# Kernel tuning notes

Hardware: AMD Instinct MI355X
Metric: run time of the kernel (lower is better)

The kernel has to match this reference:

```python
import jax, jax.numpy as jnp
import numpy as np

N_NODES = 100000
N_EDGES = 1600000
IN_FEATS = 128
HIDDEN = 150
NUM_OUT = 128


def setup_inputs() -> dict:
    key = jax.random.key(0)
    ks = jax.random.split(key, 9)
    x = jax.random.normal(ks[0], (N_NODES, IN_FEATS), dtype=jnp.float32)
    src = jax.random.randint(ks[1], (N_EDGES,), 0, N_NODES, dtype=jnp.int32)
    dst = jax.random.randint(ks[2], (N_EDGES,), 0, N_NODES, dtype=jnp.int32)
    def lin(k, fan_in, fan_out):
        bound = 1.0 / np.sqrt(fan_in)
        return jax.random.uniform(k, (fan_in, fan_out), jnp.float32, -bound, bound)
    W_self1 = lin(ks[3], IN_FEATS, HIDDEN)
    W_neigh1 = lin(ks[4], IN_FEATS, HIDDEN)
    b1 = jnp.zeros((HIDDEN,), jnp.float32)
    W_self2 = lin(ks[5], HIDDEN, NUM_OUT)
    W_neigh2 = lin(ks[6], HIDDEN, NUM_OUT)
    b2 = jnp.zeros((NUM_OUT,), jnp.float32)
    return {"x": x, "src": src, "dst": dst,
            "W_self1": W_self1, "W_neigh1": W_neigh1, "b1": b1,
            "W_self2": W_self2, "W_neigh2": W_neigh2, "b2": b2}


def _mean_agg(h, src, dst, deg_inv):
    # segment-mean of source features onto destination nodes; isolated nodes -> 0
    summed = jax.ops.segment_sum(h[src], dst, num_segments=N_NODES)
    return summed * deg_inv[:, None]


def _sage_conv(h, src, dst, deg_inv, W_self, W_neigh, b):
    h_neigh = _mean_agg(h, src, dst, deg_inv)
    return h @ W_self + h_neigh @ W_neigh + b


def reference(x, src, dst, W_self1, W_neigh1, b1, W_self2, W_neigh2, b2):
    deg = jax.ops.segment_sum(jnp.ones((src.shape[0],), x.dtype), dst,
                              num_segments=N_NODES)
    deg_inv = jnp.where(deg > 0, 1.0 / jnp.maximum(deg, 1.0), 0.0)
    h = _sage_conv(x, src, dst, deg_inv, W_self1, W_neigh1, b1)
    h = jax.nn.relu(h)
    h = _sage_conv(h, src, dst, deg_inv, W_self2, W_neigh2, b2)
    return h
```

## Files before the change

kernel.cpp:

```cpp
#include <hip/hip_runtime.h>

#define NN 100000
#define NE 1600000
#define INF 128
#define HID 150
#define NOUT 128

#define NBK 196
#define WGS 400
#define EPW 4000
#define CNTL (NBK * WGS)
#define CAP2 10240

typedef __attribute__((ext_vector_type(8))) short bf16x8;
typedef __attribute__((ext_vector_type(8))) unsigned short u16x8;
typedef __attribute__((ext_vector_type(4))) float f32x4;
typedef __attribute__((ext_vector_type(2))) float f32x2;

__device__ inline unsigned short f2bf(float f) {
    unsigned int u = __float_as_uint(f);
    u += 0x7fffu + ((u >> 16) & 1u);
    return (unsigned short)(u >> 16);
}
__device__ inline float bflo(unsigned int t) { return __uint_as_float(t << 16); }
__device__ inline float bfhi(unsigned int t) { return __uint_as_float(t & 0xffff0000u); }


__global__ __launch_bounds__(256) void sort1(const int* __restrict__ src,
                                             const int* __restrict__ dst,
                                             unsigned int* __restrict__ chunkw,
                                             int* __restrict__ cntm,
                                             int* __restrict__ segsta) {
    __shared__ int hist[NBK];
    __shared__ int off[NBK];
    __shared__ int s[256];
    __shared__ unsigned int buf[EPW];
    int w = blockIdx.x, tid = threadIdx.x;
    int e0 = w * EPW;
    for (int i = tid; i < NBK; i += 256) hist[i] = 0;
    __syncthreads();
    for (int i = tid; i < EPW; i += 256) atomicAdd(&hist[dst[e0 + i] >> 9], 1);
    __syncthreads();
    int v = (tid < NBK) ? hist[tid] : 0;
    s[tid] = v;
    __syncthreads();
    for (int o = 1; o < 256; o <<= 1) {
        int t = (tid >= o) ? s[tid - o] : 0;
        __syncthreads();
        s[tid] += t;
        __syncthreads();
    }
    if (tid < NBK) {
        int ex = s[tid] - v;
        off[tid] = ex;
        cntm[tid * WGS + w] = v;
        segsta[tid * WGS + w] = ex;
    }
    __syncthreads();
    for (int i = tid; i < EPW; i += 256) {
        int d = dst[e0 + i];
        int b = d >> 9;
        int p = atomicAdd(&off[b], 1);
        buf[p] = (unsigned int)src[e0 + i] | ((unsigned int)(d & 511) << 17);
    }
    __syncthreads();
    for (int i = tid; i < EPW; i += 256) chunkw[e0 + i] = buf[i];
}

__global__ void scanA(const int* __restrict__ in, int* __restrict__ excl,
                      int* __restrict__ blk_sums, int L) {
    __shared__ int s[256];
    int i = blockIdx.x * 256 + threadIdx.x;
    int d = (i < L) ? in[i] : 0;
    s[threadIdx.x] = d;
    __syncthreads();
    for (int o = 1; o < 256; o <<= 1) {
        int t = (threadIdx.x >= o) ? s[threadIdx.x - o] : 0;
        __syncthreads();
        s[threadIdx.x] += t;
        __syncthreads();
    }
    int incl = s[threadIdx.x];
    if (i < L) excl[i] = incl - d;
    if (threadIdx.x == 255) blk_sums[blockIdx.x] = incl;
}

__global__ void scanB(int* __restrict__ blk_sums, int nb) {
    __shared__ int s[512];
    int t = threadIdx.x;
    int v = (t < nb) ? blk_sums[t] : 0;
    s[t] = v;
    __syncthreads();
    for (int o = 1; o < 512; o <<= 1) {
        int u = (t >= o) ? s[t - o] : 0;
        __syncthreads();
        s[t] += u;
        __syncthreads();
    }
    if (t < nb) blk_sums[t] = s[t] - v;
}

__global__ void scanC(int* __restrict__ excl, const int* __restrict__ blk_sums, int L) {
    int i = blockIdx.x * 256 + threadIdx.x;
    if (i < L) excl[i] += blk_sums[blockIdx.x];
}

__global__ __launch_bounds__(256) void buildcsr2(const unsigned int* __restrict__ chunkw,
                                                 const int* __restrict__ cntm,
                                                 const int* __restrict__ segsta,
                                                 const int* __restrict__ offm,
                                                 int* __restrict__ csr_ptr,
                                                 float* __restrict__ deg_inv,
                                                 int* __restrict__ csr_src) {
    __shared__ int cnt[512];
    __shared__ int excl[512];
    __shared__ int off[512];
    __shared__ int s[256];
    __shared__ int span[CAP2];
    int b = blockIdx.x, tid = threadIdx.x;
    int base = offm[b * WGS];
    int nxt = (b == NBK - 1) ? NE : offm[(b + 1) * WGS];
    int n = nxt - base;
    if (n > CAP2) n = CAP2;
    for (int i = tid; i < 512; i += 256) cnt[i] = 0;
    __syncthreads();
    for (int sg = tid; sg < WGS; sg += 256) {
        int c = cntm[b * WGS + sg];
        int st = sg * EPW + segsta[b * WGS + sg];
        for (int j = 0; j < c; j++) atomicAdd(&cnt[chunkw[st + j] >> 17], 1);
    }
    __syncthreads();
    int a0 = cnt[2 * tid], a1 = cnt[2 * tid + 1];
    int ps = a0 + a1;
    s[tid] = ps;
    __syncthreads();
    for (int o = 1; o < 256; o <<= 1) {
        int t = (tid >= o) ? s[tid - o] : 0;
        __syncthreads();
        s[tid] += t;
        __syncthreads();
    }
    int ex = s[tid] - ps;
    excl[2 * tid] = ex;
    excl[2 * tid + 1] = ex + a0;
    off[2 * tid] = ex;
    off[2 * tid + 1] = ex + a0;
    __syncthreads();
    for (int l = tid; l < 512; l += 256) {
        int g = b * 512 + l;
        if (g < NN) {
            csr_ptr[g] = base + excl[l];
            int d = cnt[l];
            deg_inv[g] = d > 0 ? 1.0f / (float)d : 0.0f;
        }
    }
    if (b == NBK - 1 && tid == 0) csr_ptr[NN] = NE;
    for (int sg = tid; sg < WGS; sg += 256) {
        int c = cntm[b * WGS + sg];
        int st = sg * EPW + segsta[b * WGS + sg];
        for (int j = 0; j < c; j++) {
            unsigned int wd = chunkw[st + j];
            int l = wd >> 17;
            int p = atomicAdd(&off[l], 1);
            if (p < CAP2) span[p] = (int)(wd & 0x1FFFFu);
        }
    }
    __syncthreads();
    for (int i = tid; i < n; i += 256) csr_src[base + i] = span[i];
}


__global__ void cast_bf16(const float* __restrict__ in, unsigned short* __restrict__ outb,
                          int n8) {
    int i = blockIdx.x * 256 + threadIdx.x;
    if (i >= n8) return;
    const f32x4* p = (const f32x4*)in;
    f32x4 v0 = __builtin_nontemporal_load(&p[(size_t)i * 2]);
    f32x4 v1 = __builtin_nontemporal_load(&p[(size_t)i * 2 + 1]);
    u16x8 o = {f2bf(v0[0]), f2bf(v0[1]), f2bf(v0[2]), f2bf(v0[3]),
               f2bf(v1[0]), f2bf(v1[1]), f2bf(v1[2]), f2bf(v1[3])};
    ((u16x8*)outb)[i] = o;
}

__global__ void pack_weights(const float* __restrict__ Ws1, const float* __restrict__ Wn1,
                             const float* __restrict__ b1,
                             const float* __restrict__ Ws2, const float* __restrict__ Wn2,
                             unsigned short* __restrict__ W1t, unsigned short* __restrict__ W2t,
                             float* __restrict__ b1p) {
    int id = blockIdx.x * 256 + threadIdx.x;
    if (id < 160 * 256) {
        int n = id >> 8, k = id & 255;
        float v = 0.f;
        if (n < HID) v = (k < 128) ? Ws1[k * HID + n] : Wn1[(k - 128) * HID + n];
        W1t[id] = f2bf(v);
    } else if (id < 160 * 256 + 256 * 160) {
        int id2 = id - 160 * 256;
        int n = id2 / 160, k = id2 - n * 160;
        float v = 0.f;
        if (k < HID) v = (n < 128) ? Ws2[k * 128 + n] : Wn2[k * 128 + (n - 128)];
        W2t[id2] = f2bf(v);
    } else if (id < 160 * 256 + 256 * 160 + 160) {
        int n = id - (160 * 256 + 256 * 160);
        b1p[n] = (n < HID) ? b1[n] : 0.f;
    }
}


#define AGG_ACC(t)                              \
    accA += (f32x2){bflo(t.x), bfhi(t.x)};      \
    accB += (f32x2){bflo(t.y), bfhi(t.y)};      \
    accC += (f32x2){bflo(t.z), bfhi(t.z)};      \
    accD += (f32x2){bflo(t.w), bfhi(t.w)};

#define AGG_BODY(FTBL)                                                 \
    int e = start;                                                     \
    for (; e + 16 <= end; e += 16) {                                   \
        int s0 = csr_src[e + rg];                                      \
        int s1 = csr_src[e + 4 + rg];                                  \
        int s2 = csr_src[e + 8 + rg];                                  \
        int s3 = csr_src[e + 12 + rg];                                 \
        uint4 t0 = FTBL[(size_t)s0 * 16 + ch];                         \
        uint4 t1 = FTBL[(size_t)s1 * 16 + ch];                         \
        uint4 t2 = FTBL[(size_t)s2 * 16 + ch];                         \
        uint4 t3 = FTBL[(size_t)s3 * 16 + ch];                         \
        AGG_ACC(t0);                                                   \
        AGG_ACC(t1);                                                   \
        AGG_ACC(t2);                                                   \
        AGG_ACC(t3);                                                   \
    }                                                                  \
    if (e + 8 <= end) {                                                \
        int s0 = csr_src[e + rg];                                      \
        int s1 = csr_src[e + 4 + rg];                                  \
        uint4 t0 = FTBL[(size_t)s0 * 16 + ch];                         \
        uint4 t1 = FTBL[(size_t)s1 * 16 + ch];                         \
        AGG_ACC(t0);                                                   \
        AGG_ACC(t1);                                                   \
        e += 8;                                                        \
    }                                                                  \
    if (e + 4 <= end) {                                                \
        int s0 = csr_src[e + rg];                                      \
        uint4 t0 = FTBL[(size_t)s0 * 16 + ch];                         \
        AGG_ACC(t0);                                                   \
        e += 4;                                                        \
    }                                                                  \
    int rem = end - e;                                                 \
    if (rem > 0) {                                                     \
        int s0 = csr_src[(rg < rem) ? (e + rg) : e];                   \
        uint4 t = FTBL[(size_t)s0 * 16 + ch];                          \
        float wt = (rg < rem) ? 1.f : 0.f;                             \
        f32x2 w2 = {wt, wt};                                           \
        accA += w2 * (f32x2){bflo(t.x), bfhi(t.x)};                    \
        accB += w2 * (f32x2){bflo(t.y), bfhi(t.y)};                    \
        accC += w2 * (f32x2){bflo(t.z), bfhi(t.z)};                    \
        accD += w2 * (f32x2){bflo(t.w), bfhi(t.w)};                    \
    }                                                                  \
    float acc0 = accA[0], acc1 = accA[1];                              \
    float acc2 = accB[0], acc3 = accB[1];                              \
    float acc4 = accC[0], acc5 = accC[1];                              \
    float acc6 = accD[0], acc7 = accD[1];                              \
    acc0 += __shfl_xor(acc0, 32); acc1 += __shfl_xor(acc1, 32);        \
    acc2 += __shfl_xor(acc2, 32); acc3 += __shfl_xor(acc3, 32);        \
    acc4 += __shfl_xor(acc4, 32); acc5 += __shfl_xor(acc5, 32);        \
    acc6 += __shfl_xor(acc6, 32); acc7 += __shfl_xor(acc7, 32);        \
    acc0 += __shfl_xor(acc0, 16); acc1 += __shfl_xor(acc1, 16);        \
    acc2 += __shfl_xor(acc2, 16); acc3 += __shfl_xor(acc3, 16);        \
    acc4 += __shfl_xor(acc4, 16); acc5 += __shfl_xor(acc5, 16);        \
    acc6 += __shfl_xor(acc6, 16); acc7 += __shfl_xor(acc7, 16);

__global__ __launch_bounds__(256) void agg_mean_q(
    const unsigned short* __restrict__ featb, const int* __restrict__ csr_ptr,
    const float* __restrict__ deg_inv, const int* __restrict__ csr_src,
    unsigned short* __restrict__ outb) {
    int wid = threadIdx.x >> 6;
    int lane = threadIdx.x & 63;
    int v = blockIdx.x * 4 + wid;
    int start = csr_ptr[v], end = csr_ptr[v + 1];
    int rg = lane >> 4, ch = lane & 15;
    const uint4* f4 = (const uint4*)featb;
    f32x2 accA = {0.f, 0.f}, accB = {0.f, 0.f};
    f32x2 accC = {0.f, 0.f}, accD = {0.f, 0.f};
    AGG_BODY(f4);
    if (lane < 16) {
        float di = deg_inv[v];
        u16x8 o = {f2bf(acc0 * di), f2bf(acc1 * di), f2bf(acc2 * di), f2bf(acc3 * di),
                   f2bf(acc4 * di), f2bf(acc5 * di), f2bf(acc6 * di), f2bf(acc7 * di)};
        ((u16x8*)outb)[(size_t)v * 16 + ch] = o;
    }
}

__global__ __launch_bounds__(256) void agg_add_q(
    const unsigned short* __restrict__ zb, const int* __restrict__ csr_ptr,
    const float* __restrict__ deg_inv, const int* __restrict__ csr_src,
    float* __restrict__ out) {
    int wid = threadIdx.x >> 6;
    int lane = threadIdx.x & 63;
    int v = blockIdx.x * 4 + wid;
    int start = csr_ptr[v], end = csr_ptr[v + 1];
    int rg = lane >> 4, ch = lane & 15;
    const uint4* f4 = (const uint4*)zb;
    f32x2 accA = {0.f, 0.f}, accB = {0.f, 0.f};
    f32x2 accC = {0.f, 0.f}, accD = {0.f, 0.f};
    AGG_BODY(f4);
    if (lane < 16) {
        float di = deg_inv[v];
        f32x4* o4 = (f32x4*)out;
        size_t base = (size_t)v * 32 + ch * 2;
        f32x4 c0 = __builtin_nontemporal_load(&o4[base]);
        f32x4 c1 = __builtin_nontemporal_load(&o4[base + 1]);
        c0[0] += acc0 * di; c0[1] += acc1 * di; c0[2] += acc2 * di; c0[3] += acc3 * di;
        c1[0] += acc4 * di; c1[1] += acc5 * di; c1[2] += acc6 * di; c1[3] += acc7 * di;
        __builtin_nontemporal_store(c0, &o4[base]);
        __builtin_nontemporal_store(c1, &o4[base + 1]);
    }
}


__global__ __launch_bounds__(256, 4) void gemm1_mfma(
    const unsigned short* __restrict__ xb, const unsigned short* __restrict__ aggb,
    const unsigned short* __restrict__ W1t, const float* __restrict__ b1p,
    unsigned short* __restrict__ h1b) {
    __shared__ __align__(16) unsigned short A_lds[64][40];
    __shared__ __align__(16) unsigned short B_lds[160][40];
    int tid = threadIdx.x;
    int m0 = blockIdx.x * 64;
    int w = tid >> 6, lane = tid & 63;
    int lrow = lane & 15, quad = lane >> 4;
    int wr = (w & 1) * 32;
    int wc = (w >> 1) * 80;
    f32x4 acc[2][5];
    #pragma unroll
    for (int r = 0; r < 2; r++)
        #pragma unroll
        for (int c = 0; c < 5; c++) acc[r][c] = (f32x4){0.f, 0.f, 0.f, 0.f};

    for (int k0 = 0; k0 < 256; k0 += 32) {
        __syncthreads();
        {
            int row = tid >> 2, ch = tid & 3;
            int gm = m0 + row, gk = k0 + ch * 8;
            u16x8 val = {0, 0, 0, 0, 0, 0, 0, 0};
            if (gm < NN) {
                const unsigned short* sp = (gk < 128)
                    ? (xb + (size_t)gm * 128 + gk)
                    : (aggb + (size_t)gm * 128 + (gk - 128));
                val = *(const u16x8*)sp;
            }
            *(u16x8*)&A_lds[row][ch * 8] = val;
        }
        #pragma unroll
        for (int i = 0; i < 3; i++) {
            int idx = tid + i * 256;
            if (idx < 640) {
                int n = idx >> 2, ch = idx & 3;
                u16x8 val = *(const u16x8*)(W1t + (size_t)n * 256 + k0 + ch * 8);
                *(u16x8*)&B_lds[n][ch * 8] = val;
            }
        }
        __syncthreads();
        bf16x8 a[2], b[5];
        #pragma unroll
        for (int r = 0; r < 2; r++)
            a[r] = *(const bf16x8*)&A_lds[wr + r * 16 + lrow][quad * 8];
        #pragma unroll
        for (int c = 0; c < 5; c++)
            b[c] = *(const bf16x8*)&B_lds[wc + c * 16 + lrow][quad * 8];
        #pragma unroll
        for (int r = 0; r < 2; r++)
            #pragma unroll
            for (int c = 0; c < 5; c++)
                acc[r][c] = __builtin_amdgcn_mfma_f32_16x16x32_bf16(a[r], b[c], acc[r][c], 0, 0, 0);
    }
    #pragma unroll
    for (int r = 0; r < 2; r++) {
        #pragma unroll
        for (int rr = 0; rr < 4; rr++) {
            int gm = m0 + wr + r * 16 + quad * 4 + rr;
            if (gm < NN) {
                #pragma unroll
                for (int c = 0; c < 5; c++) {
                    int gn = wc + c * 16 + lrow;
                    float val = acc[r][c][rr] + b1p[gn];
                    val = val > 0.f ? val : 0.f;
                    h1b[(size_t)gm * 160 + gn] = f2bf(val);
                }
            }
        }
    }
}

__global__ __launch_bounds__(256, 4) void gemm2_mfma(
    const unsigned short* __restrict__ h1b, const unsigned short* __restrict__ W2t,
    const float* __restrict__ b2, float* __restrict__ out,
    unsigned short* __restrict__ zb) {
    __shared__ __align__(16) unsigned short A_lds[64][40];
    __shared__ __align__(16) unsigned short B_lds[128][40];
    int tid = threadIdx.x;
    int m0 = blockIdx.x * 64;
    int n0 = blockIdx.y * 128;
    int w = tid >> 6, lane = tid & 63;
    int lrow = lane & 15, quad = lane >> 4;
    int wr = (w & 1) * 32;
    int wc = (w >> 1) * 64;
    f32x4 acc[2][4];
    #pragma unroll
    for (int r = 0; r < 2; r++)
        #pragma unroll
        for (int c = 0; c < 4; c++) acc[r][c] = (f32x4){0.f, 0.f, 0.f, 0.f};

    for (int k0 = 0; k0 < 160; k0 += 32) {
        __syncthreads();
        {
            int row = tid >> 2, ch = tid & 3;
            int gm = m0 + row;
            u16x8 val = {0, 0, 0, 0, 0, 0, 0, 0};
            if (gm < NN) val = *(const u16x8*)(h1b + (size_t)gm * 160 + k0 + ch * 8);
            *(u16x8*)&A_lds[row][ch * 8] = val;
        }
        #pragma unroll
        for (int i = 0; i < 2; i++) {
            int idx = tid + i * 256;
            int n = idx >> 2, ch = idx & 3;
            u16x8 val = *(const u16x8*)(W2t + (size_t)(n0 + n) * 160 + k0 + ch * 8);
            *(u16x8*)&B_lds[n][ch * 8] = val;
        }
        __syncthreads();
        bf16x8 a[2], b[4];
        #pragma unroll
        for (int r = 0; r < 2; r++)
            a[r] = *(const bf16x8*)&A_lds[wr + r * 16 + lrow][quad * 8];
        #pragma unroll
        for (int c = 0; c < 4; c++)
            b[c] = *(const bf16x8*)&B_lds[wc + c * 16 + lrow][quad * 8];
        #pragma unroll
        for (int r = 0; r < 2; r++)
            #pragma unroll
            for (int c = 0; c < 4; c++)
                acc[r][c] = __builtin_amdgcn_mfma_f32_16x16x32_bf16(a[r], b[c], acc[r][c], 0, 0, 0);
    }
    #pragma unroll
    for (int r = 0; r < 2; r++) {
        #pragma unroll
        for (int rr = 0; rr < 4; rr++) {
            int gm = m0 + wr + r * 16 + quad * 4 + rr;
            if (gm < NN) {
                #pragma unroll
                for (int c = 0; c < 4; c++) {
                    int gn = wc + c * 16 + lrow;
                    float val = acc[r][c][rr];
                    if (n0 == 0) {
                        out[(size_t)gm * 128 + gn] = val + b2[gn];
                    } else {
                        zb[(size_t)gm * 128 + gn] = f2bf(val);
                    }
                }
            }
        }
    }
}


extern "C" void kernel_launch(void* const* d_in, const int* in_sizes, int n_in,
                              void* d_out, int out_size, void* d_ws, size_t ws_size,
                              hipStream_t stream) {
    const float* x   = (const float*)d_in[0];
    const int* src   = (const int*)d_in[1];
    const int* dst   = (const int*)d_in[2];
    const float* Ws1 = (const float*)d_in[3];
    const float* Wn1 = (const float*)d_in[4];
    const float* b1  = (const float*)d_in[5];
    const float* Ws2 = (const float*)d_in[6];
    const float* Wn2 = (const float*)d_in[7];
    const float* b2  = (const float*)d_in[8];
    float* out = (float*)d_out;

    char* p = (char*)d_ws;
    auto carve = [&](size_t bytes) {
        void* r = (void*)p;
        p += (bytes + 255) & ~(size_t)255;
        return r;
    };
    int*   csr_ptr  = (int*)carve((size_t)(NN + 1) * 4);
    float* deg_inv  = (float*)carve((size_t)NN * 4);
    int*   csr_src  = (int*)carve((size_t)NE * 4);
    int*   cntm     = (int*)carve((size_t)CNTL * 4);
    int*   offm     = (int*)carve((size_t)CNTL * 4);
    int*   segsta   = (int*)carve((size_t)CNTL * 4);
    int*   blk2     = (int*)carve(512 * 4);
    unsigned short* xb   = (unsigned short*)carve((size_t)NN * 128 * 2);
    unsigned short* aggb = (unsigned short*)carve((size_t)NN * 128 * 2);
    unsigned short* zb   = (unsigned short*)carve((size_t)NN * 128 * 2);
    unsigned short* W1t  = (unsigned short*)carve(160 * 256 * 2);
    unsigned short* W2t  = (unsigned short*)carve(256 * 160 * 2);
    float* b1p           = (float*)carve(160 * 4);
    unsigned short* h1b  = (unsigned short*)carve((size_t)NN * 160 * 2);
    unsigned int* chunkw = (unsigned int*)h1b;

    sort1<<<WGS, 256, 0, stream>>>(src, dst, chunkw, cntm, segsta);
    const int SB = (CNTL + 255) / 256;
    scanA<<<SB, 256, 0, stream>>>(cntm, offm, blk2, CNTL);
    scanB<<<1, 512, 0, stream>>>(blk2, SB);
    scanC<<<SB, 256, 0, stream>>>(offm, blk2, CNTL);
    buildcsr2<<<NBK, 256, 0, stream>>>(chunkw, cntm, segsta, offm,
                                       csr_ptr, deg_inv, csr_src);

    cast_bf16<<<(NN * 128 / 8 + 255) / 256, 256, 0, stream>>>(x, xb, NN * 128 / 8);
    pack_weights<<<(160 * 256 + 256 * 160 + 160 + 255) / 256, 256, 0, stream>>>(
        Ws1, Wn1, b1, Ws2, Wn2, W1t, W2t, b1p);

    agg_mean_q<<<NN / 4, 256, 0, stream>>>(xb, csr_ptr, deg_inv, csr_src, aggb);
    gemm1_mfma<<<dim3((NN + 63) / 64, 1), 256, 0, stream>>>(xb, aggb, W1t, b1p, h1b);

    gemm2_mfma<<<dim3((NN + 63) / 64, 2), 256, 0, stream>>>(h1b, W2t, b2, out, zb);
    agg_add_q<<<NN / 4, 256, 0, stream>>>(zb, csr_ptr, deg_inv, csr_src, out);

    (void)in_sizes; (void)n_in; (void)out_size; (void)ws_size;
}
```

Baseline: 355.2 us.

## Load MFMA operands directly from global memory instead of staging through LDS

Both GEMM kernels drop the shared-memory tiles and barriers and load A and B fragments straight from global memory into registers in MFMA layout. The K loops are fully unrolled and the occupancy hint in launch_bounds is removed. The aim is to cut LDS round-trips and __syncthreads stalls in small-K GEMMs. In exchange, each wave now fetches its own copy of overlapping A rows and weight rows, which leans on L1/L2 to serve the duplicated traffic, and register use may rise.

```diff
diff --git a/kernel.cpp b/kernel.cpp
--- a/kernel.cpp
+++ b/kernel.cpp
@@ -315,12 +315,10 @@
 }
 
 
-__global__ __launch_bounds__(256, 4) void gemm1_mfma(
+__global__ __launch_bounds__(256) void gemm1_mfma(
     const unsigned short* __restrict__ xb, const unsigned short* __restrict__ aggb,
     const unsigned short* __restrict__ W1t, const float* __restrict__ b1p,
     unsigned short* __restrict__ h1b) {
-    __shared__ __align__(16) unsigned short A_lds[64][40];
-    __shared__ __align__(16) unsigned short B_lds[160][40];
     int tid = threadIdx.x;
     int m0 = blockIdx.x * 64;
     int w = tid >> 6, lane = tid & 63;
@@ -333,37 +331,25 @@
         #pragma unroll
         for (int c = 0; c < 5; c++) acc[r][c] = (f32x4){0.f, 0.f, 0.f, 0.f};
 
+    #pragma unroll
     for (int k0 = 0; k0 < 256; k0 += 32) {
-        __syncthreads();
-        {
-            int row = tid >> 2, ch = tid & 3;
-            int gm = m0 + row, gk = k0 + ch * 8;
-            u16x8 val = {0, 0, 0, 0, 0, 0, 0, 0};
+        bf16x8 a[2], b[5];
+        #pragma unroll
+        for (int r = 0; r < 2; r++) {
+            int gm = m0 + wr + r * 16 + lrow;
+            int gk = k0 + quad * 8;
             if (gm < NN) {
                 const unsigned short* sp = (gk < 128)
                     ? (xb + (size_t)gm * 128 + gk)
                     : (aggb + (size_t)gm * 128 + (gk - 128));
-                val = *(const u16x8*)sp;
+                a[r] = *(const bf16x8*)sp;
+            } else {
+                a[r] = (bf16x8){0, 0, 0, 0, 0, 0, 0, 0};
             }
-            *(u16x8*)&A_lds[row][ch * 8] = val;
-        }
-        #pragma unroll
-        for (int i = 0; i < 3; i++) {
-            int idx = tid + i * 256;
-            if (idx < 640) {
-                int n = idx >> 2, ch = idx & 3;
-                u16x8 val = *(const u16x8*)(W1t + (size_t)n * 256 + k0 + ch * 8);
-                *(u16x8*)&B_lds[n][ch * 8] = val;
-            }
-        }
-        __syncthreads();
-        bf16x8 a[2], b[5];
-        #pragma unroll
-        for (int r = 0; r < 2; r++)
-            a[r] = *(const bf16x8*)&A_lds[wr + r * 16 + lrow][quad * 8];
+        }
         #pragma unroll
         for (int c = 0; c < 5; c++)
-            b[c] = *(const bf16x8*)&B_lds[wc + c * 16 + lrow][quad * 8];
+            b[c] = *(const bf16x8*)(W1t + (size_t)(wc + c * 16 + lrow) * 256 + k0 + quad * 8);
         #pragma unroll
         for (int r = 0; r < 2; r++)
             #pragma unroll
@@ -388,12 +374,10 @@
     }
 }
 
-__global__ __launch_bounds__(256, 4) void gemm2_mfma(
+__global__ __launch_bounds__(256) void gemm2_mfma(
     const unsigned short* __restrict__ h1b, const unsigned short* __restrict__ W2t,
     const float* __restrict__ b2, float* __restrict__ out,
     unsigned short* __restrict__ zb) {
-    __shared__ __align__(16) unsigned short A_lds[64][40];
-    __shared__ __align__(16) unsigned short B_lds[128][40];
     int tid = threadIdx.x;
     int m0 = blockIdx.x * 64;
     int n0 = blockIdx.y * 128;
@@ -407,30 +391,19 @@
         #pragma unroll
         for (int c = 0; c < 4; c++) acc[r][c] = (f32x4){0.f, 0.f, 0.f, 0.f};
 
+    #pragma unroll
     for (int k0 = 0; k0 < 160; k0 += 32) {
-        __syncthreads();
-        {
-            int row = tid >> 2, ch = tid & 3;
-            int gm = m0 + row;
-            u16x8 val = {0, 0, 0, 0, 0, 0, 0, 0};
-            if (gm < NN) val = *(const u16x8*)(h1b + (size_t)gm * 160 + k0 + ch * 8);
-            *(u16x8*)&A_lds[row][ch * 8] = val;
-        }
-        #pragma unroll
-        for (int i = 0; i < 2; i++) {
-            int idx = tid + i * 256;
-            int n = idx >> 2, ch = idx & 3;
-            u16x8 val = *(const u16x8*)(W2t + (size_t)(n0 + n) * 160 + k0 + ch * 8);
-            *(u16x8*)&B_lds[n][ch * 8] = val;
-        }
-        __syncthreads();
         bf16x8 a[2], b[4];
         #pragma unroll
-        for (int r = 0; r < 2; r++)
-            a[r] = *(const bf16x8*)&A_lds[wr + r * 16 + lrow][quad * 8];
+        for (int r = 0; r < 2; r++) {
+            int gm = m0 + wr + r * 16 + lrow;
+            a[r] = (gm < NN)
+                ? *(const bf16x8*)(h1b + (size_t)gm * 160 + k0 + quad * 8)
+                : (bf16x8){0, 0, 0, 0, 0, 0, 0, 0};
+        }
         #pragma unroll
         for (int c = 0; c < 4; c++)
-            b[c] = *(const bf16x8*)&B_lds[wc + c * 16 + lrow][quad * 8];
+            b[c] = *(const bf16x8*)(W2t + (size_t)(n0 + wc + c * 16 + lrow) * 160 + k0 + quad * 8);
         #pragma unroll
         for (int r = 0; r < 2; r++)
             #pragma unroll
```

Result: slower. 387.4 us (+9.1%).
